# Kernel tuning notes

Hardware: AMD Instinct MI355X
Metric: run time of the kernel (lower is better)

The kernel has to match this reference:

```python
import jax, jax.numpy as jnp
import numpy as np

B, S, H = 1, 2048, 1024          # batch, seq_len, hidden_dim
E, I = 16, 512                    # num_experts, moe_intermediate_size
TOP_K = 4
NORM_TOPK_PROB = True


def setup_inputs() -> dict:
    key = jax.random.key(0)
    k0, k1, k2, k3, k4 = jax.random.split(key, 5)
    scale = 0.02
    return {
        "hidden_states": jax.random.normal(k0, (B, S, H), jnp.float32),
        "w_gate": jax.random.normal(k1, (H, E), jnp.float32) * scale,
        "w_gate_proj": jax.random.normal(k2, (E, H, I), jnp.float32) * scale,
        "w_up_proj": jax.random.normal(k3, (E, H, I), jnp.float32) * scale,
        "w_down_proj": jax.random.normal(k4, (E, I, H), jnp.float32) * scale,
    }


def reference(hidden_states, w_gate, w_gate_proj, w_up_proj, w_down_proj):
    b, s, h = hidden_states.shape
    x = hidden_states.reshape(-1, h)                      # [T, H]
    T = x.shape[0]

    router_logits = x @ w_gate                            # [T, E]
    routing_weights = jax.nn.softmax(router_logits.astype(jnp.float32), axis=-1)
    top_w, sel = jax.lax.top_k(routing_weights, TOP_K)    # [T, K]
    if NORM_TOPK_PROB:
        top_w = top_w / top_w.sum(axis=-1, keepdims=True)
    top_w = top_w.astype(x.dtype)

    # Per-token combine weight for every expert (0 if not in top-k).
    # Mathematically identical to the sort/gather/index_add dispatch loop.
    combine = jnp.zeros((T, E), x.dtype).at[
        jnp.arange(T)[:, None], sel].set(top_w)           # [T, E]

    def expert_step(acc, inp):
        wg, wu, wd, w = inp                               # [H,I],[H,I],[I,H],[T]
        hidden = jax.nn.silu(x @ wg) * (x @ wu)           # [T, I]
        return acc + (hidden @ wd) * w[:, None], None

    out0 = jnp.zeros_like(x)
    out, _ = jax.lax.scan(
        expert_step, out0,
        (w_gate_proj, w_up_proj, w_down_proj, combine.T))
    return out.reshape(b, s, h), router_logits
```

## Files before the change

kernel.cpp:

```cpp
#include <hip/hip_runtime.h>
#include <math.h>

constexpr int TT = 2048;
constexpr int HH = 1024;
constexpr int EE = 16;
constexpr int II = 512;

typedef unsigned short u16;
typedef short s16x8 __attribute__((ext_vector_type(8)));
typedef float f32x4 __attribute__((ext_vector_type(4)));

__device__ __forceinline__ u16 f2bf(float f) {
  unsigned u = __float_as_uint(f);
  u = (u + 0x7fffu + ((u >> 16) & 1u)) >> 16;
  return (u16)u;
}
__device__ __forceinline__ float bf2f(u16 b) {
  return __uint_as_float(((unsigned)b) << 16);
}

__device__ __forceinline__ void gl2lds16(const void* g, void* l) {
  __builtin_amdgcn_global_load_lds(
      (const __attribute__((address_space(1))) unsigned*)g,
      (__attribute__((address_space(3))) unsigned*)l, 16, 0, 0);
}

__device__ __forceinline__ void tr4(float4& v, int li) {
  float t, r;
  t = (li & 1) ? v.x : v.y; r = __shfl_xor(t, 1);
  if (li & 1) v.x = r; else v.y = r;
  t = (li & 1) ? v.z : v.w; r = __shfl_xor(t, 1);
  if (li & 1) v.z = r; else v.w = r;
  t = (li & 2) ? v.x : v.z; r = __shfl_xor(t, 2);
  if (li & 2) v.x = r; else v.z = r;
  t = (li & 2) ? v.y : v.w; r = __shfl_xor(t, 2);
  if (li & 2) v.y = r; else v.w = r;
}

__global__ __launch_bounds__(256) void prep_kernel(
    const float* __restrict__ wgp, const float* __restrict__ wup,
    const float* __restrict__ wdp, u16* __restrict__ wgt,
    u16* __restrict__ wut, u16* __restrict__ wdt,
    const float* __restrict__ x, u16* __restrict__ xb,
    const float* __restrict__ wg, float* __restrict__ wgT) {
  int bid = blockIdx.x;
  int tid = threadIdx.x;
  if (bid < 12288) {
    int z = bid >> 8, lb = bid & 255;
    int e = z & 15, t = z >> 4;
    const float* src; u16* dst; int K, N;
    if (t == 0)      { src = wgp + (size_t)e * HH * II; dst = wgt + (size_t)e * II * HH; K = HH; N = II; }
    else if (t == 1) { src = wup + (size_t)e * HH * II; dst = wut + (size_t)e * II * HH; K = HH; N = II; }
    else             { src = wdp + (size_t)e * II * HH; dst = wdt + (size_t)e * HH * II; K = II; N = HH; }
    int nTiles = N >> 5;
    int n0 = (lb % nTiles) * 32;
    int k0 = (lb / nTiles) * 64;
    int wv = tid >> 6, l = tid & 63;
    int li = l & 3, q = l >> 2;
    int kq = k0 + wv * 16 + 8 * (q & 1);
    int nq = n0 + 4 * (q >> 1);
    float4 a = *reinterpret_cast<const float4*>(&src[(size_t)(kq + li) * N + nq]);
    float4 b = *reinterpret_cast<const float4*>(&src[(size_t)(kq + 4 + li) * N + nq]);
    tr4(a, li);
    tr4(b, li);
    uint4 st;
    st.x = (unsigned)f2bf(a.x) | ((unsigned)f2bf(a.y) << 16);
    st.y = (unsigned)f2bf(a.z) | ((unsigned)f2bf(a.w) << 16);
    st.z = (unsigned)f2bf(b.x) | ((unsigned)f2bf(b.y) << 16);
    st.w = (unsigned)f2bf(b.z) | ((unsigned)f2bf(b.w) << 16);
    *reinterpret_cast<uint4*>(&dst[(size_t)(nq + li) * K + kq]) = st;
  } else if (bid < 12288 + 2048) {
    int i = (bid - 12288) * 256 + tid;
    float4 v = reinterpret_cast<const float4*>(x)[i];
    ushort4 o;
    o.x = f2bf(v.x); o.y = f2bf(v.y); o.z = f2bf(v.z); o.w = f2bf(v.w);
    reinterpret_cast<ushort4*>(xb)[i] = o;
  } else {
    int i = (bid - 12288 - 2048) * 256 + tid;
    int h = i >> 4, e = i & 15;
    wgT[e * HH + h] = wg[i];
  }
}

__global__ void router_kernel(const float* __restrict__ x, const float* __restrict__ wgT,
                              float* __restrict__ rl, unsigned* __restrict__ selmask,
                              float* __restrict__ wsel) {
  int lane = threadIdx.x & 63, wv = threadIdx.x >> 6;
  int t = blockIdx.x * 4 + wv;
  const float* xr = x + (size_t)t * HH;
  float xv[16];
#pragma unroll
  for (int i = 0; i < 16; ++i) xv[i] = xr[lane + 64 * i];
  float lg[16];
#pragma unroll
  for (int e = 0; e < 16; ++e) {
    const float* wr = wgT + (size_t)e * HH;
    float p = 0.f;
#pragma unroll
    for (int i = 0; i < 16; ++i) p += xv[i] * wr[lane + 64 * i];
#pragma unroll
    for (int s = 32; s > 0; s >>= 1) p += __shfl_xor(p, s, 64);
    lg[e] = p;
  }
  if (lane < 16) rl[(size_t)t * 16 + lane] = lg[lane];
  unsigned mask = 0;
  int sel[4]; float bl[4];
#pragma unroll
  for (int k = 0; k < 4; ++k) {
    float best = -3.4e38f; int bi = 0;
#pragma unroll
    for (int e = 0; e < 16; ++e) {
      bool ok = !((mask >> e) & 1u) && (lg[e] > best);
      best = ok ? lg[e] : best;
      bi = ok ? e : bi;
    }
    mask |= 1u << bi;
    sel[k] = bi; bl[k] = best;
  }
  float mx = bl[0];
  float wk[4]; float s = 0.f;
#pragma unroll
  for (int k = 0; k < 4; ++k) { wk[k] = expf(bl[k] - mx); s += wk[k]; }
  float inv = 1.f / s;
  if (lane == 0) {
    selmask[t] = (unsigned)sel[0] | ((unsigned)sel[1] << 4) |
                 ((unsigned)sel[2] << 8) | ((unsigned)sel[3] << 12);
    float4 w4 = make_float4(wk[0] * inv, wk[1] * inv, wk[2] * inv, wk[3] * inv);
    reinterpret_cast<float4*>(wsel)[t] = w4;
  }
}

__global__ void build_lists_kernel(const unsigned* __restrict__ selmask,
                                   const float* __restrict__ wsel,
                                   int* __restrict__ counts, int* __restrict__ offsets,
                                   int* __restrict__ tlist, float* __restrict__ wlist,
                                   int* __restrict__ rowof) {
  __shared__ int scnt[16];
  __shared__ int soff[16];
  int lane = threadIdx.x & 63, e = threadIdx.x >> 6;
  int base = 0;
  for (int t0 = 0; t0 < TT; t0 += 64) {
    unsigned m = selmask[t0 + lane];
    bool hit = false;
#pragma unroll
    for (int j = 0; j < 4; ++j)
      hit |= (((m >> (4 * j)) & 15u) == (unsigned)e);
    base += (int)__popcll(__ballot(hit));
  }
  if (lane == 0) scnt[e] = base;
  __syncthreads();
  if (threadIdx.x == 0) {
    int s = 0;
    for (int i = 0; i < 16; ++i) { counts[i] = scnt[i]; offsets[i] = s; soff[i] = s; s += scnt[i]; }
    offsets[16] = s;
  }
  __syncthreads();
  int hb = soff[e];
  base = 0;
  for (int t0 = 0; t0 < TT; t0 += 64) {
    int t = t0 + lane;
    unsigned m = selmask[t];
    int k = -1;
#pragma unroll
    for (int j = 0; j < 4; ++j)
      if (((m >> (4 * j)) & 15u) == (unsigned)e) k = j;
    unsigned long long bal = __ballot(k >= 0);
    int pos = base + (int)__popcll(bal & ((1ull << lane) - 1ull));
    if (k >= 0) {
      tlist[e * TT + pos] = t;
      wlist[e * TT + pos] = wsel[t * 4 + k];
      rowof[t * 4 + k] = hb + pos;
    }
    base += (int)__popcll(bal);
  }
}

__global__ __launch_bounds__(256, 2) void gateup_kernel(
    const u16* __restrict__ xb, const u16* __restrict__ wgt, const u16* __restrict__ wut,
    const int* __restrict__ counts, const int* __restrict__ offsets,
    const int* __restrict__ tlist, const float* __restrict__ wlist,
    u16* __restrict__ hidden) {
  int e = blockIdx.z, mt = blockIdx.y, nt = blockIdx.x;
  int cnt = counts[e];
  if (mt * 128 >= cnt) return;
  __shared__ u16 As[128 * 64];
  __shared__ u16 Bg[64 * 64];
  __shared__ u16 Bu[64 * 64];
  int tid = threadIdx.x, lane = tid & 63, wv = tid >> 6;
  int wm = wv >> 1, wn = wv & 1;
  int srow = lane >> 3;
  int scol = (((lane & 7) ^ srow)) * 8;
  const u16* wgE = wgt + (size_t)e * II * HH;
  const u16* wuE = wut + (size_t)e * II * HH;
  const u16* gp[8];
#pragma unroll
  for (int c = 0; c < 8; ++c) {
    int chunk = c * 4 + wv;
    const u16* p;
    if (chunk < 16) {
      int mi = mt * 128 + chunk * 8 + srow; if (mi >= cnt) mi = cnt - 1;
      int tok = tlist[e * TT + mi];
      p = xb + (size_t)tok * HH + scol;
    } else if (chunk < 24) {
      int n = nt * 64 + (chunk - 16) * 8 + srow;
      p = wgE + (size_t)n * HH + scol;
    } else {
      int n = nt * 64 + (chunk - 24) * 8 + srow;
      p = wuE + (size_t)n * HH + scol;
    }
    gp[c] = p;
  }
  f32x4 accG[4][2] = {}; f32x4 accU[4][2] = {};
  int quad = lane >> 4, colc = lane & 15;
  for (int k0 = 0; k0 < HH; k0 += 64) {
#pragma unroll
    for (int c = 0; c < 8; ++c) {
      int chunk = c * 4 + wv;
      u16* dst = (chunk < 16) ? &As[chunk * 512]
               : (chunk < 24) ? &Bg[(chunk - 16) * 512]
                              : &Bu[(chunk - 24) * 512];
      gl2lds16(gp[c] + k0, dst);
    }
    __syncthreads();
#pragma unroll
    for (int kk = 0; kk < 64; kk += 32) {
      int gl = (kk >> 3) + quad;
      s16x8 a[4], bg[2], bu[2];
#pragma unroll
      for (int f = 0; f < 4; ++f) {
        int m = wm * 64 + f * 16 + colc;
        a[f] = *reinterpret_cast<const s16x8*>(&As[m * 64 + ((gl ^ (m & 7)) << 3)]);
      }
#pragma unroll
      for (int f = 0; f < 2; ++f) {
        int n = wn * 32 + f * 16 + colc;
        bg[f] = *reinterpret_cast<const s16x8*>(&Bg[n * 64 + ((gl ^ (n & 7)) << 3)]);
        bu[f] = *reinterpret_cast<const s16x8*>(&Bu[n * 64 + ((gl ^ (n & 7)) << 3)]);
      }
#pragma unroll
      for (int fm = 0; fm < 4; ++fm)
#pragma unroll
        for (int fn = 0; fn < 2; ++fn) {
          accG[fm][fn] = __builtin_amdgcn_mfma_f32_16x16x32_bf16(a[fm], bg[fn], accG[fm][fn], 0, 0, 0);
          accU[fm][fn] = __builtin_amdgcn_mfma_f32_16x16x32_bf16(a[fm], bu[fn], accU[fm][fn], 0, 0, 0);
        }
    }
    __syncthreads();
  }
  int hb = offsets[e];
#pragma unroll
  for (int fm = 0; fm < 4; ++fm) {
#pragma unroll
    for (int r = 0; r < 4; ++r) {
      int mi = mt * 128 + wm * 64 + fm * 16 + quad * 4 + r;
      if (mi < cnt) {
        float wr = wlist[e * TT + mi];
        u16* hrow = hidden + (size_t)(hb + mi) * II + nt * 64 + wn * 32;
#pragma unroll
        for (int fn = 0; fn < 2; ++fn) {
          float g = accG[fm][fn][r], u = accU[fm][fn][r];
          float hval = wr * u * g / (1.f + expf(-g));
          hrow[fn * 16 + colc] = f2bf(hval);
        }
      }
    }
  }
}

__global__ __launch_bounds__(256, 2) void down_kernel(
    const u16* __restrict__ hidden, const u16* __restrict__ wdt,
    const int* __restrict__ counts, const int* __restrict__ offsets,
    u16* __restrict__ dtmp) {
  int e = blockIdx.z, mt = blockIdx.y, nt = blockIdx.x;
  int cnt = counts[e];
  if (mt * 128 >= cnt) return;
  int hb = offsets[e];
  __shared__ u16 As[128 * 64];
  __shared__ u16 Bs[128 * 64];
  int tid = threadIdx.x, lane = tid & 63, wv = tid >> 6;
  int wm = wv >> 1, wn = wv & 1;
  int srow = lane >> 3;
  int scol = (((lane & 7) ^ srow)) * 8;
  const u16* wdE = wdt + (size_t)e * HH * II;
  const u16* gA[4]; const u16* gB[4];
#pragma unroll
  for (int c = 0; c < 4; ++c) {
    int chunk = c * 4 + wv;
    int row = hb + mt * 128 + chunk * 8 + srow;
    if (row > 8191) row = 8191;
    gA[c] = hidden + (size_t)row * II + scol;
    int n = nt * 128 + chunk * 8 + srow;
    gB[c] = wdE + (size_t)n * II + scol;
  }
  f32x4 acc[4][4] = {};
  int quad = lane >> 4, colc = lane & 15;
  for (int k0 = 0; k0 < II; k0 += 64) {
#pragma unroll
    for (int c = 0; c < 4; ++c) {
      int chunk = c * 4 + wv;
      gl2lds16(gA[c] + k0, &As[chunk * 512]);
      gl2lds16(gB[c] + k0, &Bs[chunk * 512]);
    }
    __syncthreads();
#pragma unroll
    for (int kk = 0; kk < 64; kk += 32) {
      int gl = (kk >> 3) + quad;
      s16x8 a[4], b[4];
#pragma unroll
      for (int f = 0; f < 4; ++f) {
        int m = wm * 64 + f * 16 + colc;
        int n = wn * 64 + f * 16 + colc;
        a[f] = *reinterpret_cast<const s16x8*>(&As[m * 64 + ((gl ^ (m & 7)) << 3)]);
        b[f] = *reinterpret_cast<const s16x8*>(&Bs[n * 64 + ((gl ^ (n & 7)) << 3)]);
      }
#pragma unroll
      for (int fm = 0; fm < 4; ++fm)
#pragma unroll
        for (int fn = 0; fn < 4; ++fn)
          acc[fm][fn] = __builtin_amdgcn_mfma_f32_16x16x32_bf16(a[fm], b[fn], acc[fm][fn], 0, 0, 0);
    }
    __syncthreads();
  }
#pragma unroll
  for (int fm = 0; fm < 4; ++fm) {
#pragma unroll
    for (int r = 0; r < 4; ++r) {
      int mi = mt * 128 + wm * 64 + fm * 16 + quad * 4 + r;
      if (mi < cnt) {
        u16* drow = dtmp + (size_t)(hb + mi) * HH + nt * 128 + wn * 64;
#pragma unroll
        for (int fn = 0; fn < 4; ++fn)
          drow[fn * 16 + colc] = f2bf(acc[fm][fn][r]);
      }
    }
  }
}

__global__ void combine_kernel(const u16* __restrict__ dtmp, const int* __restrict__ rowof,
                               float* __restrict__ out) {
  int t = blockIdx.x, tid = threadIdx.x;
  int4 rw = reinterpret_cast<const int4*>(rowof)[t];
  int h = tid * 4;
  float s0 = 0.f, s1 = 0.f, s2 = 0.f, s3 = 0.f;
  int rows[4] = {rw.x, rw.y, rw.z, rw.w};
#pragma unroll
  for (int k = 0; k < 4; ++k) {
    ushort4 v = *reinterpret_cast<const ushort4*>(&dtmp[(size_t)rows[k] * HH + h]);
    s0 += bf2f(v.x); s1 += bf2f(v.y); s2 += bf2f(v.z); s3 += bf2f(v.w);
  }
  *reinterpret_cast<float4*>(&out[(size_t)t * HH + h]) = make_float4(s0, s1, s2, s3);
}

extern "C" void kernel_launch(void* const* d_in, const int* in_sizes, int n_in,
                              void* d_out, int out_size, void* d_ws, size_t ws_size,
                              hipStream_t stream) {
  const float* x   = (const float*)d_in[0];
  const float* wg  = (const float*)d_in[1];
  const float* wgp = (const float*)d_in[2];
  const float* wup = (const float*)d_in[3];
  const float* wdp = (const float*)d_in[4];
  float* out = (float*)d_out;
  float* rl  = out + (size_t)TT * HH;

  char* w = (char*)d_ws;
  int*      counts  = (int*)(w + 0);
  int*      offsets = (int*)(w + 64);
  unsigned* selmask = (unsigned*)(w + 1024);
  float*    wsel    = (float*)(w + 16384);
  int*      rowof   = (int*)(w + 49152);
  int*      tlist   = (int*)(w + 81920);
  float*    wlist   = (float*)(w + 210944);
  float*    wgT     = (float*)(w + 339968);
  u16*      xb      = (u16*)(w + 405504);
  u16*      wgt     = xb  + (size_t)TT * HH;
  u16*      wut     = wgt + (size_t)EE * II * HH;
  u16*      wdt     = wut + (size_t)EE * II * HH;
  u16*      hidden  = wdt + (size_t)EE * HH * II;
  u16*      dtmp    = wgt;

  hipLaunchKernelGGL(prep_kernel, dim3(12288 + 2048 + 64), dim3(256), 0, stream,
                     wgp, wup, wdp, wgt, wut, wdt, x, xb, wg, wgT);
  hipLaunchKernelGGL(router_kernel, dim3(TT / 4), dim3(256), 0, stream,
                     x, wgT, rl, selmask, wsel);
  hipLaunchKernelGGL(build_lists_kernel, dim3(1), dim3(1024), 0, stream,
                     selmask, wsel, counts, offsets, tlist, wlist, rowof);
  hipLaunchKernelGGL(gateup_kernel, dim3(8, 16, 16), dim3(256), 0, stream,
                     xb, wgt, wut, counts, offsets, tlist, wlist, hidden);
  hipLaunchKernelGGL(down_kernel, dim3(8, 16, 16), dim3(256), 0, stream,
                     hidden, wdt, counts, offsets, dtmp);
  hipLaunchKernelGGL(combine_kernel, dim3(TT), dim3(256), 0, stream,
                     dtmp, rowof, out);
}
```

Before: 240.9 us.

## Fuse expert weight bf16 conversion and transpose into GEMM B-tile staging

```diff
diff --git a/kernel.cpp b/kernel.cpp
--- a/kernel.cpp
+++ b/kernel.cpp
@@ -37,46 +37,33 @@
   if (li & 2) v.y = r; else v.w = r;
 }
 
-__global__ __launch_bounds__(256) void prep_kernel(
-    const float* __restrict__ wgp, const float* __restrict__ wup,
-    const float* __restrict__ wdp, u16* __restrict__ wgt,
-    u16* __restrict__ wut, u16* __restrict__ wdt,
-    const float* __restrict__ x, u16* __restrict__ xb,
-    const float* __restrict__ wg, float* __restrict__ wgT) {
-  int bid = blockIdx.x;
-  int tid = threadIdx.x;
-  if (bid < 12288) {
-    int z = bid >> 8, lb = bid & 255;
-    int e = z & 15, t = z >> 4;
-    const float* src; u16* dst; int K, N;
-    if (t == 0)      { src = wgp + (size_t)e * HH * II; dst = wgt + (size_t)e * II * HH; K = HH; N = II; }
-    else if (t == 1) { src = wup + (size_t)e * HH * II; dst = wut + (size_t)e * II * HH; K = HH; N = II; }
-    else             { src = wdp + (size_t)e * II * HH; dst = wdt + (size_t)e * HH * II; K = II; N = HH; }
-    int nTiles = N >> 5;
-    int n0 = (lb % nTiles) * 32;
-    int k0 = (lb / nTiles) * 64;
-    int wv = tid >> 6, l = tid & 63;
-    int li = l & 3, q = l >> 2;
-    int kq = k0 + wv * 16 + 8 * (q & 1);
-    int nq = n0 + 4 * (q >> 1);
-    float4 a = *reinterpret_cast<const float4*>(&src[(size_t)(kq + li) * N + nq]);
-    float4 b = *reinterpret_cast<const float4*>(&src[(size_t)(kq + 4 + li) * N + nq]);
-    tr4(a, li);
-    tr4(b, li);
-    uint4 st;
-    st.x = (unsigned)f2bf(a.x) | ((unsigned)f2bf(a.y) << 16);
-    st.y = (unsigned)f2bf(a.z) | ((unsigned)f2bf(a.w) << 16);
-    st.z = (unsigned)f2bf(b.x) | ((unsigned)f2bf(b.y) << 16);
-    st.w = (unsigned)f2bf(b.z) | ((unsigned)f2bf(b.w) << 16);
-    *reinterpret_cast<uint4*>(&dst[(size_t)(nq + li) * K + kq]) = st;
-  } else if (bid < 12288 + 2048) {
-    int i = (bid - 12288) * 256 + tid;
+__device__ __forceinline__ void stageB(const float* __restrict__ src, int ldn,
+                                       int krow, int ncol, int g, u16* lds,
+                                       int li, int q) {
+  const float* p = src + (size_t)krow * ldn + ncol + 4 * q;
+  float4 a = *reinterpret_cast<const float4*>(p);
+  float4 b = *reinterpret_cast<const float4*>(p + 4 * ldn);
+  tr4(a, li); tr4(b, li);
+  uint4 st;
+  st.x = (unsigned)f2bf(a.x) | ((unsigned)f2bf(a.y) << 16);
+  st.y = (unsigned)f2bf(a.z) | ((unsigned)f2bf(a.w) << 16);
+  st.z = (unsigned)f2bf(b.x) | ((unsigned)f2bf(b.y) << 16);
+  st.w = (unsigned)f2bf(b.z) | ((unsigned)f2bf(b.w) << 16);
+  int n = 4 * q + li;
+  *reinterpret_cast<uint4*>(&lds[n * 64 + ((g ^ (n & 7)) << 3)]) = st;
+}
+
+__global__ void prep_kernel(const float* __restrict__ x, u16* __restrict__ xb,
+                            const float* __restrict__ wg, float* __restrict__ wgT) {
+  int b = blockIdx.x;
+  if (b < 2048) {
+    int i = b * 256 + threadIdx.x;
     float4 v = reinterpret_cast<const float4*>(x)[i];
     ushort4 o;
     o.x = f2bf(v.x); o.y = f2bf(v.y); o.z = f2bf(v.z); o.w = f2bf(v.w);
     reinterpret_cast<ushort4*>(xb)[i] = o;
   } else {
-    int i = (bid - 12288 - 2048) * 256 + tid;
+    int i = (b - 2048) * 256 + threadIdx.x;
     int h = i >> 4, e = i & 15;
     wgT[e * HH + h] = wg[i];
   }
@@ -176,7 +163,7 @@
 }
 
 __global__ __launch_bounds__(256, 2) void gateup_kernel(
-    const u16* __restrict__ xb, const u16* __restrict__ wgt, const u16* __restrict__ wut,
+    const u16* __restrict__ xb, const float* __restrict__ wgp, const float* __restrict__ wup,
     const int* __restrict__ counts, const int* __restrict__ offsets,
     const int* __restrict__ tlist, const float* __restrict__ wlist,
     u16* __restrict__ hidden) {
@@ -190,36 +177,30 @@
   int wm = wv >> 1, wn = wv & 1;
   int srow = lane >> 3;
   int scol = (((lane & 7) ^ srow)) * 8;
-  const u16* wgE = wgt + (size_t)e * II * HH;
-  const u16* wuE = wut + (size_t)e * II * HH;
-  const u16* gp[8];
-#pragma unroll
-  for (int c = 0; c < 8; ++c) {
+  int li = lane & 3, q = lane >> 2;
+  const float* wgE = wgp + (size_t)e * HH * II;
+  const float* wuE = wup + (size_t)e * HH * II;
+  const u16* gA[4];
+#pragma unroll
+  for (int c = 0; c < 4; ++c) {
     int chunk = c * 4 + wv;
-    const u16* p;
-    if (chunk < 16) {
-      int mi = mt * 128 + chunk * 8 + srow; if (mi >= cnt) mi = cnt - 1;
-      int tok = tlist[e * TT + mi];
-      p = xb + (size_t)tok * HH + scol;
-    } else if (chunk < 24) {
-      int n = nt * 64 + (chunk - 16) * 8 + srow;
-      p = wgE + (size_t)n * HH + scol;
-    } else {
-      int n = nt * 64 + (chunk - 24) * 8 + srow;
-      p = wuE + (size_t)n * HH + scol;
-    }
-    gp[c] = p;
+    int mi = mt * 128 + chunk * 8 + srow; if (mi >= cnt) mi = cnt - 1;
+    int tok = tlist[e * TT + mi];
+    gA[c] = xb + (size_t)tok * HH + scol;
   }
   f32x4 accG[4][2] = {}; f32x4 accU[4][2] = {};
   int quad = lane >> 4, colc = lane & 15;
   for (int k0 = 0; k0 < HH; k0 += 64) {
 #pragma unroll
-    for (int c = 0; c < 8; ++c) {
-      int chunk = c * 4 + wv;
-      u16* dst = (chunk < 16) ? &As[chunk * 512]
-               : (chunk < 24) ? &Bg[(chunk - 16) * 512]
-                              : &Bu[(chunk - 24) * 512];
-      gl2lds16(gp[c] + k0, dst);
+    for (int c = 0; c < 4; ++c)
+      gl2lds16(gA[c] + k0, &As[(c * 4 + wv) * 512]);
+#pragma unroll
+    for (int p = 0; p < 4; ++p) {
+      int unit = wv * 4 + p;
+      int g = unit & 7;
+      const float* src = (unit >> 3) ? wuE : wgE;
+      u16* lds = (unit >> 3) ? Bu : Bg;
+      stageB(src, II, k0 + g * 8 + li, nt * 64, g, lds, li, q);
     }
     __syncthreads();
 #pragma unroll
@@ -268,7 +249,7 @@
 }
 
 __global__ __launch_bounds__(256, 2) void down_kernel(
-    const u16* __restrict__ hidden, const u16* __restrict__ wdt,
+    const u16* __restrict__ hidden, const float* __restrict__ wdp,
     const int* __restrict__ counts, const int* __restrict__ offsets,
     u16* __restrict__ dtmp) {
   int e = blockIdx.z, mt = blockIdx.y, nt = blockIdx.x;
@@ -281,25 +262,28 @@
   int wm = wv >> 1, wn = wv & 1;
   int srow = lane >> 3;
   int scol = (((lane & 7) ^ srow)) * 8;
-  const u16* wdE = wdt + (size_t)e * HH * II;
-  const u16* gA[4]; const u16* gB[4];
+  int li = lane & 3, q = lane >> 2;
+  const float* wdE = wdp + (size_t)e * II * HH;
+  const u16* gA[4];
 #pragma unroll
   for (int c = 0; c < 4; ++c) {
     int chunk = c * 4 + wv;
     int row = hb + mt * 128 + chunk * 8 + srow;
     if (row > 8191) row = 8191;
     gA[c] = hidden + (size_t)row * II + scol;
-    int n = nt * 128 + chunk * 8 + srow;
-    gB[c] = wdE + (size_t)n * II + scol;
   }
   f32x4 acc[4][4] = {};
   int quad = lane >> 4, colc = lane & 15;
   for (int k0 = 0; k0 < II; k0 += 64) {
 #pragma unroll
-    for (int c = 0; c < 4; ++c) {
-      int chunk = c * 4 + wv;
-      gl2lds16(gA[c] + k0, &As[chunk * 512]);
-      gl2lds16(gB[c] + k0, &Bs[chunk * 512]);
+    for (int c = 0; c < 4; ++c)
+      gl2lds16(gA[c] + k0, &As[(c * 4 + wv) * 512]);
+#pragma unroll
+    for (int p = 0; p < 4; ++p) {
+      int unit = wv * 4 + p;
+      int g = unit & 7;
+      int nb = unit >> 3;
+      stageB(wdE, HH, k0 + g * 8 + li, nt * 128 + nb * 64, g, &Bs[nb * 64 * 64], li, q);
     }
     __syncthreads();
 #pragma unroll
@@ -372,22 +356,19 @@
   float*    wlist   = (float*)(w + 210944);
   float*    wgT     = (float*)(w + 339968);
   u16*      xb      = (u16*)(w + 405504);
-  u16*      wgt     = xb  + (size_t)TT * HH;
-  u16*      wut     = wgt + (size_t)EE * II * HH;
-  u16*      wdt     = wut + (size_t)EE * II * HH;
-  u16*      hidden  = wdt + (size_t)EE * HH * II;
-  u16*      dtmp    = wgt;
-
-  hipLaunchKernelGGL(prep_kernel, dim3(12288 + 2048 + 64), dim3(256), 0, stream,
-                     wgp, wup, wdp, wgt, wut, wdt, x, xb, wg, wgT);
+  u16*      hidden  = xb + (size_t)TT * HH;
+  u16*      dtmp    = hidden + (size_t)4 * TT * II;
+
+  hipLaunchKernelGGL(prep_kernel, dim3(2048 + 64), dim3(256), 0, stream,
+                     x, xb, wg, wgT);
   hipLaunchKernelGGL(router_kernel, dim3(TT / 4), dim3(256), 0, stream,
                      x, wgT, rl, selmask, wsel);
   hipLaunchKernelGGL(build_lists_kernel, dim3(1), dim3(1024), 0, stream,
                      selmask, wsel, counts, offsets, tlist, wlist, rowof);
   hipLaunchKernelGGL(gateup_kernel, dim3(8, 16, 16), dim3(256), 0, stream,
-                     xb, wgt, wut, counts, offsets, tlist, wlist, hidden);
+                     xb, wgp, wup, counts, offsets, tlist, wlist, hidden);
   hipLaunchKernelGGL(down_kernel, dim3(8, 16, 16), dim3(256), 0, stream,
-                     hidden, wdt, counts, offsets, dtmp);
+                     hidden, wdp, counts, offsets, dtmp);
   hipLaunchKernelGGL(combine_kernel, dim3(TT), dim3(256), 0, stream,
                      dtmp, rowof, out);
 }
```

After: 265.5 us. 1.1x slower.
